# Performance work log

Measured on AMD Instinct MI355X. Metric: run time of the kernel, lower is better.

## Reference

```python
import jax, jax.numpy as jnp
import numpy as np

B, S, D, H, DK, DV, DO = 2, 2048, 1024, 16, 64, 64, 1024


def setup_inputs() -> dict:
    key = jax.random.key(0)
    k0, k1, k2, k3, k4 = jax.random.split(key, 5)
    x = jax.random.normal(k0, (B, S, D), dtype=jnp.float32)
    # Stacked per-head projection weights (original uses H separate Linear(bias=False));
    # stored as [H, D, d_head] so q = x @ Wq[h] per head.
    Wq = jax.random.normal(k1, (H, D, DK), dtype=jnp.float32) * 0.02
    Wk = jax.random.normal(k2, (H, D, DK), dtype=jnp.float32) * 0.02
    Wv = jax.random.normal(k3, (H, D, DV), dtype=jnp.float32) * 0.02
    # Output projection Linear(dim_v*num_heads, dim_out, bias=False), stored [H*DV, DO]
    Wo = jax.random.normal(k4, (H * DV, DO), dtype=jnp.float32) * 0.02
    return {"x": x, "Wq": Wq, "Wk": Wk, "Wv": Wv, "Wo": Wo}


def reference(x, Wq, Wk, Wv, Wo):
    # Cross-head batched version of the per-head Python loop (same math).
    q = jnp.einsum('bsd,hde->bhse', x, Wq)  # [B,H,S,DK]
    k = jnp.einsum('bsd,hde->bhse', x, Wk)  # [B,H,S,DK]
    v = jnp.einsum('bsd,hde->bhse', x, Wv)  # [B,H,S,DV]
    scale = 1.0 / jnp.sqrt(jnp.asarray(k.shape[-1], dtype=x.dtype))
    scores = jnp.einsum('bhqe,bhke->bhqk', q, k) * scale  # [B,H,S,S]
    attn = jax.nn.softmax(scores, axis=-1)
    o = jnp.einsum('bhqk,bhke->bhqe', attn, v)  # [B,H,S,DV]
    # concat heads along feature dim (head order preserved)
    o = jnp.transpose(o, (0, 2, 1, 3)).reshape(o.shape[0], o.shape[2], -1)  # [B,S,H*DV]
    return o @ Wo  # [B,S,DO]
```

## Files before the change

kernel.cpp:

```cpp
#include <hip/hip_runtime.h>

typedef __bf16 bf16;
typedef __attribute__((ext_vector_type(8))) short short8;
typedef __attribute__((ext_vector_type(4))) short short4v;
typedef __attribute__((ext_vector_type(4))) float floatx4;
typedef __attribute__((ext_vector_type(16))) float floatx16;

#define DEVINL __device__ __forceinline__

DEVINL void gll16(const void* g, void* l) {
  __builtin_amdgcn_global_load_lds((const __attribute__((address_space(1))) void*)g,
                                   (__attribute__((address_space(3))) void*)l, 16, 0, 0);
}

DEVINL float fast_exp2(float x) { return __builtin_amdgcn_exp2f(x); }

#define QSCALE 0.18033688011112042f

__global__ __launch_bounds__(256) void prep_all(const float* __restrict__ x,
                                                const float* __restrict__ Wq,
                                                const float* __restrict__ Wk,
                                                const float* __restrict__ Wv,
                                                const float* __restrict__ Wo,
                                                bf16* __restrict__ x_bf,
                                                bf16* __restrict__ WbigT,
                                                bf16* __restrict__ WoT) {
  __shared__ float tile[64][65];
  int bid = blockIdx.x;
  if (bid < 2048) {
    int i = (bid * 256 + threadIdx.x) * 8;
    float4 a = *(const float4*)(x + i);
    float4 b = *(const float4*)(x + i + 4);
    union { bf16 h[8]; short8 s; } u;
    u.h[0] = (bf16)a.x; u.h[1] = (bf16)a.y; u.h[2] = (bf16)a.z; u.h[3] = (bf16)a.w;
    u.h[4] = (bf16)b.x; u.h[5] = (bf16)b.y; u.h[6] = (bf16)b.z; u.h[7] = (bf16)b.w;
    *(short8*)(x_bf + i) = u.s;
    return;
  }
  int t = bid - 2048;
  int which = t >> 8;
  t &= 255;
  const float* in;
  bf16* out;
  int C, tilesC, tilesPerBatch;
  long inStride;
  if (which < 3) {
    in = which == 0 ? Wq : (which == 1 ? Wk : Wv);
    out = WbigT + (long)which * 1024 * 1024;
    C = 64; tilesC = 1; tilesPerBatch = 16; inStride = 65536;
  } else {
    in = Wo; out = WoT;
    C = 1024; tilesC = 16; tilesPerBatch = 256; inStride = 0;
  }
  int batch = t / tilesPerBatch;
  int tt = t % tilesPerBatch;
  int ri = tt / tilesC, ci = tt % tilesC;
  const float* src = in + batch * inStride;
  bf16* dst = out + batch * (long)65536 * (which < 3 ? 1 : 0);
  int tx = threadIdx.x & 63, ty = threadIdx.x >> 6;
#pragma unroll
  for (int i = 0; i < 16; i++) {
    int r = ty + i * 4;
    tile[r][tx] = src[(long)(ri * 64 + r) * C + ci * 64 + tx];
  }
  __syncthreads();
#pragma unroll
  for (int i = 0; i < 16; i++) {
    int c = ty + i * 4;
    dst[(long)(ci * 64 + c) * 1024 + ri * 64 + tx] = (bf16)tile[tx][c];
  }
}

__global__ __launch_bounds__(512, 2) void gemm256_qkv(const bf16* __restrict__ A,
                                                      const bf16* __restrict__ BT,
                                                      bf16* __restrict__ q_ws,
                                                      bf16* __restrict__ k_ws,
                                                      bf16* __restrict__ v_ws) {
  extern __shared__ char lds[];
  int swz = (blockIdx.x & 7) * 24 + (blockIdx.x >> 3);
  int bm = swz / 12, bn = swz % 12;
  int tid = threadIdx.x, lane = tid & 63, wid = tid >> 6;
  int wm = wid >> 2, wn = wid & 3;
  int ql = lane & 15, g = lane >> 4;
  int sw = (ql & 7) << 4;
  int hB = wn >> 1;
  char* ldsA = lds;
  char* ldsB = lds + 65536;

  const char* Abase = (const char*)A + (long)bm * 256 * 2048;
  const char* Bbase = (const char*)BT + (long)bn * 256 * 2048;
  int scb = ((tid & 7) * 16) ^ (((tid >> 3) & 7) << 4);

  floatx4 acc[8][4] = {};
  short8 aF[4], bF[4];

#define STG(dst0, src0, kt_, h_) do {                                              \
    _Pragma("unroll") for (int j_ = 0; j_ < 2; j_++)                               \
      gll16((src0) + (long)((h_) * 128 + j_ * 64 + (tid >> 3)) * 2048              \
                   + (kt_) * 128 + scb,                                            \
            (dst0) + ((kt_) & 1) * 32768 + (h_) * 16384 + j_ * 8192 + wid * 1024); \
  } while (0)
#define LDA(slot_, frh_, kk_) do {                                                 \
    _Pragma("unroll") for (int j_ = 0; j_ < 4; j_++)                               \
      aF[j_] = *(const short8*)(ldsA + (slot_) * 32768 + wm * 16384 +              \
               (((frh_) * 4 + j_) * 16 + ql) * 128 + (((kk_) * 64 + g * 16) ^ sw));\
  } while (0)
#define LDB(slot_, kk_) do {                                                       \
    _Pragma("unroll") for (int f_ = 0; f_ < 4; f_++)                               \
      bF[f_] = *(const short8*)(ldsB + (slot_) * 32768 + hB * 16384 +              \
               ((wn & 1) * 64 + f_ * 16 + ql) * 128 + (((kk_) * 64 + g * 16) ^ sw));\
  } while (0)
#define MFMA16(frh_) do {                                                          \
    __builtin_amdgcn_s_setprio(1);                                                 \
    _Pragma("unroll") for (int j_ = 0; j_ < 4; j_++)                               \
      _Pragma("unroll") for (int f_ = 0; f_ < 4; f_++)                             \
        acc[(frh_) * 4 + j_][f_] = __builtin_amdgcn_mfma_f32_16x16x32_bf16(        \
            aF[j_], bF[f_], acc[(frh_) * 4 + j_][f_], 0, 0, 0);                    \
    __builtin_amdgcn_s_setprio(0);                                                 \
  } while (0)
#define BAR __builtin_amdgcn_s_barrier()
#define LG0 asm volatile("s_waitcnt lgkmcnt(0)" ::: "memory")

  STG(ldsB, Bbase, 0, 0); STG(ldsB, Bbase, 0, 1);
  STG(ldsA, Abase, 0, 0); STG(ldsA, Abase, 0, 1);
  STG(ldsB, Bbase, 1, 0);

  for (int it = 0; it < 8; it++) {
    int b1 = 2 * it + 1, a2 = 2 * it + 2, b2 = 2 * it + 3;
    bool more = it < 7;
    asm volatile("s_waitcnt vmcnt(2)" ::: "memory");
    BAR;
    LDA(0, 0, 0); LDB(0, 0);
    STG(ldsA, Abase, b1, 0);
    BAR; LG0; MFMA16(0); BAR;
    LDA(0, 1, 0);
    STG(ldsA, Abase, b1, 1);
    BAR; LG0; MFMA16(1); BAR;
    LDA(0, 0, 1); LDB(0, 1);
    STG(ldsB, Bbase, b1, 1);
    BAR; LG0; MFMA16(0); BAR;
    LDA(0, 1, 1);
    if (more) STG(ldsB, Bbase, a2, 0);
    BAR; LG0; MFMA16(1); BAR;
    if (more) { asm volatile("s_waitcnt vmcnt(2)" ::: "memory"); }
    else      { asm volatile("s_waitcnt vmcnt(0)" ::: "memory"); }
    BAR;
    LDA(1, 0, 0); LDB(1, 0);
    if (more) STG(ldsB, Bbase, a2, 1);
    BAR; LG0; MFMA16(0); BAR;
    LDA(1, 1, 0);
    if (more) STG(ldsA, Abase, a2, 0);
    BAR; LG0; MFMA16(1); BAR;
    LDA(1, 0, 1); LDB(1, 1);
    if (more) STG(ldsA, Abase, a2, 1);
    BAR; LG0; MFMA16(0); BAR;
    LDA(1, 1, 1);
    if (more) STG(ldsB, Bbase, b2, 0);
    BAR; LG0; MFMA16(1); BAR;
  }
#undef STG
#undef LDA
#undef LDB
#undef MFMA16
#undef BAR
#undef LG0

  if (bn < 8) {
    bf16* dst = (bn < 4) ? q_ws : k_ws;
    float scale = (bn < 4) ? QSCALE : 1.0f;
#pragma unroll
    for (int fr = 0; fr < 8; fr++)
#pragma unroll
      for (int fc = 0; fc < 4; fc++)
#pragma unroll
        for (int i = 0; i < 4; i++) {
          int r = bm * 256 + wm * 128 + fr * 16 + g * 4 + i;
          int c = bn * 256 + wn * 64 + fc * 16 + ql;
          int b = r >> 11, s = r & 2047;
          int h = (c >> 6) & 15, e = c & 63;
          long bh = (long)b * 16 + h;
          dst[(bh * 2048 + s) * 64 + e] = (bf16)(acc[fr][fc][i] * scale);
        }
  } else {
#pragma unroll
    for (int fr = 0; fr < 8; fr++)
#pragma unroll
      for (int fc = 0; fc < 4; fc++) {
        int local_c = wn * 64 + fc * 16 + ql;
        int ls0 = wm * 128 + fr * 16 + g * 4;
        int sp = (ls0 & ~12) | ((ls0 & 4) << 1) | ((ls0 & 8) >> 1);
        union { bf16 hh[4]; short4v s4; } u;
#pragma unroll
        for (int i = 0; i < 4; i++) u.hh[i] = (bf16)acc[fr][fc][i];
        *(short4v*)(lds + local_c * 512 + ((sp * 2) ^ ((local_c & 7) << 4))) = u.s4;
      }
    __syncthreads();
    int b = bm >> 3;
    long sbase = (long)(bm & 7) * 256;
#pragma unroll
    for (int j = 0; j < 16; j++) {
      int local_c = wid * 32 + j * 2 + (lane >> 5);
      int chunk = lane & 31;
      int cg = bn * 256 + local_c;
      int h = (cg >> 6) & 15, e = cg & 63;
      long bh = (long)b * 16 + h;
      char* dstp = (char*)v_ws + ((bh * 64 + e) * 2048 + sbase) * 2 + chunk * 16;
      *(short8*)dstp = *(const short8*)(lds + local_c * 512 + ((chunk * 16) ^ ((local_c & 7) << 4)));
    }
  }
}

__global__ __launch_bounds__(256) void gemm_out(const bf16* __restrict__ A,
                                                const bf16* __restrict__ BT,
                                                float* __restrict__ Cout,
                                                int N, int gridN) {
  int cpx = gridDim.x >> 3;
  int swz = (blockIdx.x & 7) * cpx + (blockIdx.x >> 3);
  int bm = swz / gridN, bn = swz % gridN;
  __shared__ char lds[65536];
  int tid = threadIdx.x;
  int lane = tid & 63, wid = tid >> 6;
  int wr = wid >> 1, wc = wid & 1;
  floatx4 acc[4][4] = {};
  const char* Abase = (const char*)A + (long)bm * 128 * 2048;
  const char* Bbase = (const char*)BT + (long)bn * 128 * 2048;
  int scb = ((tid & 7) * 16) ^ (((tid >> 3) & 7) << 4);

#define OSTG(kt_) do {                                                             \
    char* la_ = lds + ((kt_) & 1) * 16384;                                         \
    char* lb_ = lds + 32768 + ((kt_) & 1) * 16384;                                 \
    _Pragma("unroll") for (int q_ = 0; q_ < 4; q_++) {                             \
      gll16(Abase + (long)(q_ * 32 + (tid >> 3)) * 2048 + (kt_) * 128 + scb,       \
            la_ + q_ * 4096 + wid * 1024);                                         \
      gll16(Bbase + (long)(q_ * 32 + (tid >> 3)) * 2048 + (kt_) * 128 + scb,       \
            lb_ + q_ * 4096 + wid * 1024);                                         \
    }                                                                              \
  } while (0)

  OSTG(0);
  for (int kt = 0; kt < 16; kt++) {
    if (kt < 15) {
      OSTG(kt + 1);
      asm volatile("s_waitcnt vmcnt(8)" ::: "memory");
    } else {
      asm volatile("s_waitcnt vmcnt(0)" ::: "memory");
    }
    __builtin_amdgcn_s_barrier();
    char* la = lds + (kt & 1) * 16384;
    char* lb = lds + 32768 + (kt & 1) * 16384;
#pragma unroll
    for (int kk = 0; kk < 2; kk++) {
      short8 a[4], b[4];
#pragma unroll
      for (int mi = 0; mi < 4; mi++) {
        int row = wr * 64 + mi * 16 + (lane & 15);
        int col = (kk * 64 + (lane >> 4) * 16) ^ ((row & 7) << 4);
        a[mi] = *(const short8*)(la + row * 128 + col);
      }
#pragma unroll
      for (int ni = 0; ni < 4; ni++) {
        int row = wc * 64 + ni * 16 + (lane & 15);
        int col = (kk * 64 + (lane >> 4) * 16) ^ ((row & 7) << 4);
        b[ni] = *(const short8*)(lb + row * 128 + col);
      }
#pragma unroll
      for (int mi = 0; mi < 4; mi++)
#pragma unroll
        for (int ni = 0; ni < 4; ni++)
          acc[mi][ni] = __builtin_amdgcn_mfma_f32_16x16x32_bf16(a[mi], b[ni], acc[mi][ni], 0, 0, 0);
    }
    __builtin_amdgcn_s_barrier();
  }
#undef OSTG

#pragma unroll
  for (int mi = 0; mi < 4; mi++)
#pragma unroll
    for (int ni = 0; ni < 4; ni++)
#pragma unroll
      for (int i = 0; i < 4; i++) {
        int r = bm * 128 + wr * 64 + mi * 16 + (lane >> 4) * 4 + i;
        int c = bn * 128 + wc * 64 + ni * 16 + (lane & 15);
        Cout[(long)r * N + c] = acc[mi][ni][i];
      }
}

__global__ __launch_bounds__(1024, 4) void attn_kernel(const bf16* __restrict__ q_ws,
                                                       const bf16* __restrict__ k_ws,
                                                       const bf16* __restrict__ v_ws,
                                                       bf16* __restrict__ obuf) {
  extern __shared__ char lds[];
  int wgid = ((blockIdx.x & 7) << 5) + (blockIdx.x >> 3);
  int qt = wgid & 7;
  int bh = wgid >> 3;
  int b = bh >> 4, hh = bh & 15;
  int tid = threadIdx.x, lane = tid & 63, wid = tid >> 6;
  int grp = wid >> 3, w8 = wid & 7;
  int l31 = lane & 31, h2 = lane >> 5;
  char* kbuf = lds + grp * 65536;
  char* vbuf = kbuf + 32768;

  const char* kbase = (const char*)k_ws + (long)bh * 2048 * 128 + (long)grp * 131072;
  const char* vbase = (const char*)v_ws + (long)bh * 64 * 4096 + (long)grp * 2048;

  int srow = w8 * 8 + (lane >> 3);
  int scb = ((lane & 7) * 16) ^ (((lane >> 3) & 7) << 4);

#define STAGE(t_) do {                                                              \
    gll16(kbase + ((long)(t_) * 64 + srow) * 128 + scb,                             \
          kbuf + ((t_) & 3) * 8192 + w8 * 1024);                                    \
    gll16(vbase + (long)srow * 4096 + (long)(t_) * 128 + scb,                       \
          vbuf + ((t_) & 3) * 8192 + w8 * 1024);                                    \
  } while (0)

#define WAIT2_BAR do {                                                              \
    asm volatile("s_waitcnt vmcnt(2)" ::: "memory");                                \
    __builtin_amdgcn_s_barrier();                                                   \
    asm volatile("" ::: "memory");                                                  \
  } while (0)

  int rofs = l31 * 128, swz = (lane & 7) << 4, h16 = h2 << 4;
  int fof[4];
#pragma unroll
  for (int m = 0; m < 4; m++) fof[m] = rofs + ((32 * m + h16) ^ swz);

  const bf16* qrow = q_ws + ((long)bh * 2048 + qt * 256 + w8 * 32 + l31) * 64 + 8 * h2;
  short8 qreg[4];
#pragma unroll
  for (int dt = 0; dt < 4; dt++) qreg[dt] = *(const short8*)(qrow + 16 * dt);

  floatx16 sa0, sa1;
  floatx16 o0 = {}, o1 = {};
  short8 pb[4];
  float ls[4] = {0.f, 0.f, 0.f, 0.f};

#define QKSTEP(kc) do {                                                             \
    __builtin_amdgcn_s_setprio(1);                                                  \
    _Pragma("unroll") for (int dt_ = 0; dt_ < 4; dt_++) {                           \
      short8 ka_ = *(const short8*)((kc) + fof[dt_]);                               \
      short8 kb_ = *(const short8*)((kc) + 4096 + fof[dt_]);                        \
      if (dt_ == 0) {                                                               \
        sa0 = __builtin_amdgcn_mfma_f32_32x32x16_bf16(ka_, qreg[0], (floatx16){}, 0, 0, 0); \
        sa1 = __builtin_amdgcn_mfma_f32_32x32x16_bf16(kb_, qreg[0], (floatx16){}, 0, 0, 0); \
      } else {                                                                      \
        sa0 = __builtin_amdgcn_mfma_f32_32x32x16_bf16(ka_, qreg[dt_], sa0, 0, 0, 0);\
        sa1 = __builtin_amdgcn_mfma_f32_32x32x16_bf16(kb_, qreg[dt_], sa1, 0, 0, 0);\
      }                                                                             \
    }                                                                               \
    __builtin_amdgcn_s_setprio(0);                                                  \
  } while (0)

#define SMSTEP do {                                                                 \
    if (__builtin_expect(ls[0] > 1e30f, 0)) {                                       \
      const float c_ = 7.8886091e-31f;                                  \
      _Pragma("unroll") for (int i_ = 0; i_ < 4; i_++) ls[i_] *= c_;                \
      _Pragma("unroll") for (int i_ = 0; i_ < 16; i_++) { o0[i_] *= c_; o1[i_] *= c_; } \
    }                                                                               \
    { union { bf16 hh_[8]; short8 s_; } u_;                                         \
      _Pragma("unroll") for (int j_ = 0; j_ < 8; j_++) {                            \
        float e_ = fast_exp2(sa0[j_]); ls[j_ & 3] += e_; u_.hh_[j_] = (bf16)e_; }   \
      pb[0] = u_.s_;                                                                \
      _Pragma("unroll") for (int j_ = 0; j_ < 8; j_++) {                            \
        float e_ = fast_exp2(sa0[8 + j_]); ls[j_ & 3] += e_; u_.hh_[j_] = (bf16)e_; } \
      pb[1] = u_.s_;                                                                \
      _Pragma("unroll") for (int j_ = 0; j_ < 8; j_++) {                            \
        float e_ = fast_exp2(sa1[j_]); ls[j_ & 3] += e_; u_.hh_[j_] = (bf16)e_; }   \
      pb[2] = u_.s_;                                                                \
      _Pragma("unroll") for (int j_ = 0; j_ < 8; j_++) {                            \
        float e_ = fast_exp2(sa1[8 + j_]); ls[j_ & 3] += e_; u_.hh_[j_] = (bf16)e_; } \
      pb[3] = u_.s_;                                                                \
    }                                                                               \
  } while (0)

#define PVSTEP(vc) do {                                                             \
    __builtin_amdgcn_s_setprio(1);                                                  \
    _Pragma("unroll") for (int c_ = 0; c_ < 4; c_++) {                              \
      short8 va_ = *(const short8*)((vc) + fof[c_]);                                \
      short8 vb_ = *(const short8*)((vc) + 4096 + fof[c_]);                         \
      o0 = __builtin_amdgcn_mfma_f32_32x32x16_bf16(va_, pb[c_], o0, 0, 0, 0);       \
      o1 = __builtin_amdgcn_mfma_f32_32x32x16_bf16(vb_, pb[c_], o1, 0, 0, 0);       \
    }                                                                               \
    __builtin_amdgcn_s_setprio(0);                                                  \
  } while (0)

  STAGE(0); STAGE(1);
  WAIT2_BAR;
  QKSTEP(kbuf + 0 * 8192);
  STAGE(2);

  for (int t = 0; t <= 12; t++) {
    SMSTEP;
    PVSTEP(vbuf + (t & 3) * 8192);
    WAIT2_BAR;
    STAGE(t + 3);
    QKSTEP(kbuf + ((t + 1) & 3) * 8192);
  }
  SMSTEP;
  PVSTEP(vbuf + (13 & 3) * 8192);
  WAIT2_BAR;
  QKSTEP(kbuf + (14 & 3) * 8192);
  SMSTEP;
  PVSTEP(vbuf + (14 & 3) * 8192);
  asm volatile("s_waitcnt vmcnt(0)" ::: "memory");
  __builtin_amdgcn_s_barrier();
  QKSTEP(kbuf + (15 & 3) * 8192);
  SMSTEP;
  PVSTEP(vbuf + (15 & 3) * 8192);

#undef STAGE
#undef WAIT2_BAR
#undef QKSTEP
#undef SMSTEP
#undef PVSTEP

  __syncthreads();
  float lsum = (ls[0] + ls[1]) + (ls[2] + ls[3]);
  float lpair = lsum + __shfl_xor(lsum, 32);
  int sq = qt * 256 + w8 * 32 + l31;
  if (grp == 1) {
    char* pk = lds + 65536 + w8 * 8192;
    *(floatx16*)(pk + lane * 64) = o0;
    *(floatx16*)(pk + 4096 + lane * 64) = o1;
    if (h2 == 0) *(float*)(lds + (w8 * 32 + l31) * 4) = lpair;
  }
  __syncthreads();
  if (grp == 0) {
    const char* pk = lds + 65536 + w8 * 8192;
    floatx16 a0 = *(const floatx16*)(pk + lane * 64);
    floatx16 a1 = *(const floatx16*)(pk + 4096 + lane * 64);
    float lp = *(const float*)(lds + (w8 * 32 + l31) * 4);
    float inv = 1.f / (lpair + lp);
    bf16* orow = obuf + ((long)b * 2048 + sq) * 1024 + hh * 64;
#pragma unroll
    for (int rg = 0; rg < 4; rg++) {
      union { bf16 hv[4]; short4v s4; } uo;
#pragma unroll
      for (int i = 0; i < 4; i++) uo.hv[i] = (bf16)((o0[4 * rg + i] + a0[4 * rg + i]) * inv);
      *(short4v*)(orow + 8 * rg + 4 * h2) = uo.s4;
#pragma unroll
      for (int i = 0; i < 4; i++) uo.hv[i] = (bf16)((o1[4 * rg + i] + a1[4 * rg + i]) * inv);
      *(short4v*)(orow + 32 + 8 * rg + 4 * h2) = uo.s4;
    }
  }
}

extern "C" void kernel_launch(void* const* d_in, const int* in_sizes, int n_in,
                              void* d_out, int out_size, void* d_ws, size_t ws_size,
                              hipStream_t stream) {
  const float* x  = (const float*)d_in[0];
  const float* Wq = (const float*)d_in[1];
  const float* Wk = (const float*)d_in[2];
  const float* Wv = (const float*)d_in[3];
  const float* Wo = (const float*)d_in[4];
  float* out = (float*)d_out;

  char* ws = (char*)d_ws;
  bf16* x_bf  = (bf16*)(ws);
  bf16* WbigT = (bf16*)(ws + 8388608);
  bf16* WoT   = (bf16*)(ws + 14680064);
  bf16* q_ws  = (bf16*)(ws + 16777216);
  bf16* k_ws  = (bf16*)(ws + 25165824);
  bf16* v_ws  = (bf16*)(ws + 33554432);
  bf16* obuf  = (bf16*)(ws + 41943040);

  hipFuncSetAttribute((const void*)gemm256_qkv,
                      hipFuncAttributeMaxDynamicSharedMemorySize, 131072);
  hipFuncSetAttribute((const void*)attn_kernel,
                      hipFuncAttributeMaxDynamicSharedMemorySize, 131072);

  prep_all<<<3072, 256, 0, stream>>>(x, Wq, Wk, Wv, Wo, x_bf, WbigT, WoT);
  gemm256_qkv<<<192, 512, 131072, stream>>>(x_bf, WbigT, q_ws, k_ws, v_ws);
  attn_kernel<<<256, 1024, 131072, stream>>>(q_ws, k_ws, v_ws, obuf);
  gemm_out<<<256, 256, 0, stream>>>(obuf, WoT, out, 1024, 8);
}
```

Before: 111.9 us.

## Halve attention workgroup size and KV tile to double grid occupancy

The attention kernel goes from 1024-thread workgroups covering 256 query rows to 512-thread workgroups covering 128 rows, launched as 512 blocks instead of 256. The KV tile per step shrinks from 64 to 32 keys, with new LDS swizzles for K and V and a 64 KB static LDS allocation. The aim is to fill more CUs and fit more workgroups per CU on a 256-CU part. In exchange there are twice as many pipeline iterations and barriers, and each K/V tile is loaded by twice as many workgroups.

Result: faster. 105.0 us (-6.1%).

```diff
diff --git a/kernel.cpp b/kernel.cpp
--- a/kernel.cpp
+++ b/kernel.cpp
@@ -285,32 +285,34 @@
       }
 }
 
-__global__ __launch_bounds__(1024, 4) void attn_kernel(const bf16* __restrict__ q_ws,
-                                                       const bf16* __restrict__ k_ws,
-                                                       const bf16* __restrict__ v_ws,
-                                                       bf16* __restrict__ obuf) {
-  extern __shared__ char lds[];
-  int wgid = ((blockIdx.x & 7) << 5) + (blockIdx.x >> 3);
-  int qt = wgid & 7;
-  int bh = wgid >> 3;
+__global__ __launch_bounds__(512, 4) void attn_kernel(const bf16* __restrict__ q_ws,
+                                                      const bf16* __restrict__ k_ws,
+                                                      const bf16* __restrict__ v_ws,
+                                                      bf16* __restrict__ obuf) {
+  __shared__ char lds[65536];
+  int wgid = ((blockIdx.x & 7) << 6) + (blockIdx.x >> 3);
+  int qt = wgid & 15;
+  int bh = wgid >> 4;
   int b = bh >> 4, hh = bh & 15;
   int tid = threadIdx.x, lane = tid & 63, wid = tid >> 6;
-  int grp = wid >> 3, w8 = wid & 7;
+  int grp = wid >> 2, w4 = wid & 3;
   int l31 = lane & 31, h2 = lane >> 5;
-  char* kbuf = lds + grp * 65536;
-  char* vbuf = kbuf + 32768;
+  char* kbuf = lds + grp * 32768;
+  char* vbuf = kbuf + 16384;
 
   const char* kbase = (const char*)k_ws + (long)bh * 2048 * 128 + (long)grp * 131072;
   const char* vbase = (const char*)v_ws + (long)bh * 64 * 4096 + (long)grp * 2048;
 
-  int srow = w8 * 8 + (lane >> 3);
-  int scb = ((lane & 7) * 16) ^ (((lane >> 3) & 7) << 4);
+  int ksrow = w4 * 8 + (lane >> 3);
+  int kscb = (((lane & 7) ^ (lane >> 3) ^ w4) << 4);
+  int vsrow = w4 * 16 + (lane >> 2);
+  int vscb = ((((lane & 3) ^ ((lane >> 3) & 3)) << 4));
 
 #define STAGE(t_) do {                                                              \
-    gll16(kbase + ((long)(t_) * 64 + srow) * 128 + scb,                             \
-          kbuf + ((t_) & 3) * 8192 + w8 * 1024);                                    \
-    gll16(vbase + (long)srow * 4096 + (long)(t_) * 128 + scb,                       \
-          vbuf + ((t_) & 3) * 8192 + w8 * 1024);                                    \
+    gll16(kbase + ((long)(t_) * 32 + ksrow) * 128 + kscb,                           \
+          kbuf + ((t_) & 3) * 4096 + w4 * 1024);                                    \
+    gll16(vbase + (long)vsrow * 4096 + (long)(t_) * 64 + vscb,                      \
+          vbuf + ((t_) & 3) * 4096 + w4 * 1024);                                    \
   } while (0)
 
 #define WAIT2_BAR do {                                                              \
@@ -319,34 +321,31 @@
     asm volatile("" ::: "memory");                                                  \
   } while (0)
 
-  int rofs = l31 * 128, swz = (lane & 7) << 4, h16 = h2 << 4;
-  int fof[4];
-#pragma unroll
-  for (int m = 0; m < 4; m++) fof[m] = rofs + ((32 * m + h16) ^ swz);
-
-  const bf16* qrow = q_ws + ((long)bh * 2048 + qt * 256 + w8 * 32 + l31) * 64 + 8 * h2;
+  int Sk = ((l31 & 7) ^ (l31 >> 3)) << 4;
+  int Sv = ((l31 >> 1) & 3) << 4;
+  int fofk[4], fofv[2];
+#pragma unroll
+  for (int dt = 0; dt < 4; dt++) fofk[dt] = l31 * 128 + ((dt * 32 + 16 * h2) ^ Sk);
+#pragma unroll
+  for (int c = 0; c < 2; c++) fofv[c] = l31 * 64 + ((c * 32 + 16 * h2) ^ Sv);
+
+  const bf16* qrow = q_ws + ((long)bh * 2048 + qt * 128 + w4 * 32 + l31) * 64 + 8 * h2;
   short8 qreg[4];
 #pragma unroll
   for (int dt = 0; dt < 4; dt++) qreg[dt] = *(const short8*)(qrow + 16 * dt);
 
-  floatx16 sa0, sa1;
+  floatx16 sa;
   floatx16 o0 = {}, o1 = {};
-  short8 pb[4];
+  short8 pb[2];
   float ls[4] = {0.f, 0.f, 0.f, 0.f};
 
 #define QKSTEP(kc) do {                                                             \
     __builtin_amdgcn_s_setprio(1);                                                  \
-    _Pragma("unroll") for (int dt_ = 0; dt_ < 4; dt_++) {                           \
-      short8 ka_ = *(const short8*)((kc) + fof[dt_]);                               \
-      short8 kb_ = *(const short8*)((kc) + 4096 + fof[dt_]);                        \
-      if (dt_ == 0) {                                                               \
-        sa0 = __builtin_amdgcn_mfma_f32_32x32x16_bf16(ka_, qreg[0], (floatx16){}, 0, 0, 0); \
-        sa1 = __builtin_amdgcn_mfma_f32_32x32x16_bf16(kb_, qreg[0], (floatx16){}, 0, 0, 0); \
-      } else {                                                                      \
-        sa0 = __builtin_amdgcn_mfma_f32_32x32x16_bf16(ka_, qreg[dt_], sa0, 0, 0, 0);\
-        sa1 = __builtin_amdgcn_mfma_f32_32x32x16_bf16(kb_, qreg[dt_], sa1, 0, 0, 0);\
-      }                                                                             \
-    }                                                                               \
+    sa = __builtin_amdgcn_mfma_f32_32x32x16_bf16(                                   \
+        *(const short8*)((kc) + fofk[0]), qreg[0], (floatx16){}, 0, 0, 0);          \
+    _Pragma("unroll") for (int dt_ = 1; dt_ < 4; dt_++)                             \
+      sa = __builtin_amdgcn_mfma_f32_32x32x16_bf16(                                 \
+          *(const short8*)((kc) + fofk[dt_]), qreg[dt_], sa, 0, 0, 0);              \
     __builtin_amdgcn_s_setprio(0);                                                  \
   } while (0)
 
@@ -358,54 +357,48 @@
     }                                                                               \
     { union { bf16 hh_[8]; short8 s_; } u_;                                         \
       _Pragma("unroll") for (int j_ = 0; j_ < 8; j_++) {                            \
-        float e_ = fast_exp2(sa0[j_]); ls[j_ & 3] += e_; u_.hh_[j_] = (bf16)e_; }   \
+        float e_ = fast_exp2(sa[j_]); ls[j_ & 3] += e_; u_.hh_[j_] = (bf16)e_; }    \
       pb[0] = u_.s_;                                                                \
       _Pragma("unroll") for (int j_ = 0; j_ < 8; j_++) {                            \
-        float e_ = fast_exp2(sa0[8 + j_]); ls[j_ & 3] += e_; u_.hh_[j_] = (bf16)e_; } \
+        float e_ = fast_exp2(sa[8 + j_]); ls[j_ & 3] += e_; u_.hh_[j_] = (bf16)e_; }\
       pb[1] = u_.s_;                                                                \
-      _Pragma("unroll") for (int j_ = 0; j_ < 8; j_++) {                            \
-        float e_ = fast_exp2(sa1[j_]); ls[j_ & 3] += e_; u_.hh_[j_] = (bf16)e_; }   \
-      pb[2] = u_.s_;                                                                \
-      _Pragma("unroll") for (int j_ = 0; j_ < 8; j_++) {                            \
-        float e_ = fast_exp2(sa1[8 + j_]); ls[j_ & 3] += e_; u_.hh_[j_] = (bf16)e_; } \
-      pb[3] = u_.s_;                                                                \
     }                                                                               \
   } while (0)
 
 #define PVSTEP(vc) do {                                                             \
     __builtin_amdgcn_s_setprio(1);                                                  \
-    _Pragma("unroll") for (int c_ = 0; c_ < 4; c_++) {                              \
-      short8 va_ = *(const short8*)((vc) + fof[c_]);                                \
-      short8 vb_ = *(const short8*)((vc) + 4096 + fof[c_]);                         \
-      o0 = __builtin_amdgcn_mfma_f32_32x32x16_bf16(va_, pb[c_], o0, 0, 0, 0);       \
-      o1 = __builtin_amdgcn_mfma_f32_32x32x16_bf16(vb_, pb[c_], o1, 0, 0, 0);       \
+    _Pragma("unroll") for (int c_ = 0; c_ < 2; c_++) {                              \
+      o0 = __builtin_amdgcn_mfma_f32_32x32x16_bf16(                                 \
+          *(const short8*)((vc) + fofv[c_]), pb[c_], o0, 0, 0, 0);                  \
+      o1 = __builtin_amdgcn_mfma_f32_32x32x16_bf16(                                 \
+          *(const short8*)((vc) + 2048 + fofv[c_]), pb[c_], o1, 0, 0, 0);           \
     }                                                                               \
     __builtin_amdgcn_s_setprio(0);                                                  \
   } while (0)
 
   STAGE(0); STAGE(1);
   WAIT2_BAR;
-  QKSTEP(kbuf + 0 * 8192);
+  QKSTEP(kbuf + 0 * 4096);
   STAGE(2);
 
-  for (int t = 0; t <= 12; t++) {
+  for (int t = 0; t <= 28; t++) {
     SMSTEP;
-    PVSTEP(vbuf + (t & 3) * 8192);
+    PVSTEP(vbuf + (t & 3) * 4096);
     WAIT2_BAR;
     STAGE(t + 3);
-    QKSTEP(kbuf + ((t + 1) & 3) * 8192);
+    QKSTEP(kbuf + ((t + 1) & 3) * 4096);
   }
   SMSTEP;
-  PVSTEP(vbuf + (13 & 3) * 8192);
+  PVSTEP(vbuf + (29 & 3) * 4096);
   WAIT2_BAR;
-  QKSTEP(kbuf + (14 & 3) * 8192);
+  QKSTEP(kbuf + (30 & 3) * 4096);
   SMSTEP;
-  PVSTEP(vbuf + (14 & 3) * 8192);
+  PVSTEP(vbuf + (30 & 3) * 4096);
   asm volatile("s_waitcnt vmcnt(0)" ::: "memory");
   __builtin_amdgcn_s_barrier();
-  QKSTEP(kbuf + (15 & 3) * 8192);
+  QKSTEP(kbuf + (31 & 3) * 4096);
   SMSTEP;
-  PVSTEP(vbuf + (15 & 3) * 8192);
+  PVSTEP(vbuf + (31 & 3) * 4096);
 
 #undef STAGE
 #undef WAIT2_BAR
@@ -416,19 +409,19 @@
   __syncthreads();
   float lsum = (ls[0] + ls[1]) + (ls[2] + ls[3]);
   float lpair = lsum + __shfl_xor(lsum, 32);
-  int sq = qt * 256 + w8 * 32 + l31;
+  int sq = qt * 128 + w4 * 32 + l31;
   if (grp == 1) {
-    char* pk = lds + 65536 + w8 * 8192;
+    char* pk = lds + 32768 + w4 * 8192;
     *(floatx16*)(pk + lane * 64) = o0;
     *(floatx16*)(pk + 4096 + lane * 64) = o1;
-    if (h2 == 0) *(float*)(lds + (w8 * 32 + l31) * 4) = lpair;
+    if (h2 == 0) *(float*)(lds + (w4 * 32 + l31) * 4) = lpair;
   }
   __syncthreads();
   if (grp == 0) {
-    const char* pk = lds + 65536 + w8 * 8192;
+    const char* pk = lds + 32768 + w4 * 8192;
     floatx16 a0 = *(const floatx16*)(pk + lane * 64);
     floatx16 a1 = *(const floatx16*)(pk + 4096 + lane * 64);
-    float lp = *(const float*)(lds + (w8 * 32 + l31) * 4);
+    float lp = *(const float*)(lds + (w4 * 32 + l31) * 4);
     float inv = 1.f / (lpair + lp);
     bf16* orow = obuf + ((long)b * 2048 + sq) * 1024 + hh * 64;
 #pragma unroll
@@ -465,11 +458,9 @@
 
   hipFuncSetAttribute((const void*)gemm256_qkv,
                       hipFuncAttributeMaxDynamicSharedMemorySize, 131072);
-  hipFuncSetAttribute((const void*)attn_kernel,
-                      hipFuncAttributeMaxDynamicSharedMemorySize, 131072);
 
   prep_all<<<3072, 256, 0, stream>>>(x, Wq, Wk, Wv, Wo, x_bf, WbigT, WoT);
   gemm256_qkv<<<192, 512, 131072, stream>>>(x_bf, WbigT, q_ws, k_ws, v_ws);
-  attn_kernel<<<256, 1024, 131072, stream>>>(q_ws, k_ws, v_ws, obuf);
+  attn_kernel<<<512, 512, 0, stream>>>(q_ws, k_ws, v_ws, obuf);
   gemm_out<<<256, 256, 0, stream>>>(obuf, WoT, out, 1024, 8);
 }
```
